# Kernel tuning notes

Hardware: AMD Instinct MI355X
Metric: run time of the kernel (lower is better)

## Reference

```python
import jax, jax.numpy as jnp
import numpy as np

S, B, D, H, DH = 1024, 4, 1024, 16, 64


def setup_inputs() -> dict:
    key = jax.random.key(0)
    ks = jax.random.split(key, 12)
    inp = {
        "query": jax.random.normal(ks[0], (S, B, D), dtype=jnp.float32),
        "key": jax.random.normal(ks[1], (S, B, D), dtype=jnp.float32),
        "value": jax.random.normal(ks[2], (S, B, D), dtype=jnp.float32),
        "key_mask": jax.random.randint(ks[3], (S, B), 0, 2, dtype=jnp.int32),
        # per-head stacked projection weights (original loops nn.Linear per head)
        "Wq": jax.random.normal(ks[4], (H, D, DH), dtype=jnp.float32) * 0.02,
        "bq": jnp.zeros((H, DH), dtype=jnp.float32),
        "Wk": jax.random.normal(ks[5], (H, D, DH), dtype=jnp.float32) * 0.02,
        "bk": jnp.zeros((H, DH), dtype=jnp.float32),
        "Wv": jax.random.normal(ks[6], (H, D, DH), dtype=jnp.float32) * 0.02,
        "bv": jnp.zeros((H, DH), dtype=jnp.float32),
        "Wo": jax.random.normal(ks[7], (H * DH, D), dtype=jnp.float32) * 0.02,
        "bo": jnp.zeros((D,), dtype=jnp.float32),
    }
    return inp


def reference(query, key, value, key_mask, Wq, bq, Wk, bk, Wv, bv, Wo, bo):
    # query/key/value: [S, B, D] (seq-major, matching torch einsum 'imk,jmk->imj')
    q = jnp.einsum('smd,hdk->smhk', query, Wq) + bq  # [Sq, B, H, DH]
    k = jnp.einsum('smd,hdk->smhk', key, Wk) + bk    # [Sk, B, H, DH]
    v = jnp.einsum('smd,hdk->smhk', value, Wv) + bv  # [Sk, B, H, DH]

    scale = 1.0 / jnp.sqrt(jnp.float32(DH))
    scores = jnp.einsum('imhk,jmhk->himj', q, k) * scale  # [H, Sq, B, Sk]
    # key_mask: [Sk, B] -> transpose -> [B, Sk]; additive -1e18 masking
    scores = scores - key_mask.astype(jnp.float32).T * 1e18
    attn = jax.nn.softmax(scores, axis=-1)
    out = jnp.einsum('himj,jmhk->imhk', attn, v)  # [Sq, B, H, DH]
    concat = out.reshape(out.shape[0], out.shape[1], H * DH)
    return concat @ Wo + bo  # [Sq, B, D]
```

## Files before the change

### kernel.cpp

```cpp
#include <hip/hip_runtime.h>
#include <hip/hip_bf16.h>


typedef __attribute__((ext_vector_type(8))) short short8;
typedef __attribute__((ext_vector_type(4))) short short4_;
typedef __attribute__((ext_vector_type(4))) float f32x4;
typedef __attribute__((ext_vector_type(16))) float f32x16;
typedef __attribute__((ext_vector_type(8))) __bf16 bf16x8;
typedef __attribute__((ext_vector_type(4))) __bf16 bf16x4;

union B8 {
    short8 s;
    bf16x8 b;
    unsigned short u[8];
};
union B4 {
    short4_ s;
    bf16x4 b;
    unsigned short u[4];
    int i[2];
};

#if __has_builtin(__builtin_amdgcn_exp2f)
#define EXP2(x) __builtin_amdgcn_exp2f(x)
#else
#define EXP2(x) exp2f(x)
#endif
#if __has_builtin(__builtin_amdgcn_rcpf)
#define RCP(x) __builtin_amdgcn_rcpf(x)
#else
#define RCP(x) (1.0f / (x))
#endif

static __device__ __forceinline__ unsigned short f2bf_rne(float f) {
    union { float f; unsigned u; } v; v.f = f;
    unsigned r = v.u + 0x7FFFu + ((v.u >> 16) & 1u);
    return (unsigned short)(r >> 16);
}

static __device__ __forceinline__ void async_lds16(const void* g, const void* l) {
    __builtin_amdgcn_global_load_lds(
        (const __attribute__((address_space(1))) unsigned int*)(unsigned long long)g,
        (__attribute__((address_space(3))) unsigned int*)(unsigned int)(unsigned long long)l,
        16, 0, 0);
}

__global__ __launch_bounds__(256) void prep(
    const float* __restrict__ Wq, const float* __restrict__ Wk,
    const float* __restrict__ Wv, const float* __restrict__ Wo,
    const float* __restrict__ query, const float* __restrict__ key,
    const float* __restrict__ value,
    unsigned short* __restrict__ WT,
    unsigned short* __restrict__ qA, unsigned short* __restrict__ kA,
    unsigned short* __restrict__ vA) {
    const int t = threadIdx.x;
    const int z = blockIdx.z;

    if (z >= 4) {
        const int zz = z - 4;
        const int tensor = zz >> 2;
        const int part = zz & 3;
        const float* src = (tensor == 0) ? query : (tensor == 1) ? key : value;
        unsigned short* dst = (tensor == 0) ? qA : (tensor == 1) ? kA : vA;
        const int blk = blockIdx.y * 16 + blockIdx.x;
        const size_t base = (size_t)part * 1048576 + (size_t)blk * 4096 + t * 16;
        B8 w0, w1;
#pragma unroll
        for (int i = 0; i < 2; ++i) {
            f32x4 a = *(const f32x4*)(src + base + i * 8);
            f32x4 b = *(const f32x4*)(src + base + i * 8 + 4);
#pragma unroll
            for (int j = 0; j < 4; ++j) {
                (i ? w1 : w0).u[j] = f2bf_rne(a[j]);
                (i ? w1 : w0).u[4 + j] = f2bf_rne(b[j]);
            }
        }
        *(short8*)(dst + base) = w0.s;
        *(short8*)(dst + base + 8) = w1.s;
        return;
    }

    __shared__ float sT[64][65];
    const int dtile = blockIdx.x;
    const int sub = blockIdx.y;
    const float* src;
    int spitch;
    unsigned short* dst;
    if (z < 3) {
        const float* W = (z == 0) ? Wq : (z == 1) ? Wk : Wv;
        src = W + (size_t)sub * 65536 + (size_t)dtile * 64 * 64;
        spitch = 64;
        dst = WT + (size_t)z * 1048576 + (size_t)(sub * 64) * 1024 + dtile * 64;
    } else {
        src = Wo + (size_t)dtile * 64 * 1024 + sub * 64;
        spitch = 1024;
        dst = WT + (size_t)3 * 1048576 + (size_t)(sub * 64) * 1024 + dtile * 64;
    }

    const int r = t >> 2;
    const int cseg = (t & 3) * 16;
#pragma unroll
    for (int i = 0; i < 4; ++i) {
        f32x4 v = *(const f32x4*)(src + (size_t)r * spitch + cseg + i * 4);
#pragma unroll
        for (int j = 0; j < 4; ++j) sT[r][cseg + i * 4 + j] = v[j];
    }
    __syncthreads();
    B8 w0, w1;
#pragma unroll
    for (int i = 0; i < 8; ++i) {
        w0.u[i] = f2bf_rne(sT[cseg + i][r]);
        w1.u[i] = f2bf_rne(sT[cseg + 8 + i][r]);
    }
    *(short8*)(dst + (size_t)r * 1024 + cseg) = w0.s;
    *(short8*)(dst + (size_t)r * 1024 + cseg + 8) = w1.s;
}

template <bool OUT_F32, bool BIAS_ROW>
__device__ __forceinline__ void gemm128(unsigned short* __restrict__ sA,
                                        unsigned short* __restrict__ sB,
                                        const unsigned short* __restrict__ A,
                                        size_t lda,
                                        const unsigned short* __restrict__ Bt,
                                        size_t ldb,
                                        const float* __restrict__ bias,
                                        void* __restrict__ Cv, size_t ldc,
                                        float oscale, int row0, int col0) {
    const int t = threadIdx.x;
    const int w = t >> 6;
    const int lane = t & 63;
    const int quad = lane >> 4;
    const int l15 = lane & 15;
    const int wr = w >> 1;
    const int wc = w & 1;
    const int srow16 = lane >> 2;
    const int sgseg = (lane & 3) ^ ((lane >> 3) & 3);
    const int rseg = (quad ^ ((l15 >> 1) & 3)) * 8;

    f32x4 acc[4][4] = {};

    const unsigned short* agp = A + (size_t)(row0 + w * 32 + srow16) * lda + sgseg * 8;
    const unsigned short* agp2 = agp + (size_t)16 * lda;
    const unsigned short* bgp = Bt + (size_t)(col0 + w * 32 + srow16) * ldb + sgseg * 8;
    const unsigned short* bgp2 = bgp + (size_t)16 * ldb;
    const int ldsA0 = (w * 32) * 32;
    const int ldsA1 = (w * 32 + 16) * 32;

    auto STAGE = [&](int tt, int off) {
        const int k0 = tt * 32;
        async_lds16(agp + k0, sA + off + ldsA0);
        async_lds16(agp2 + k0, sA + off + ldsA1);
        async_lds16(bgp + k0, sB + off + ldsA0);
        async_lds16(bgp2 + k0, sB + off + ldsA1);
    };
    auto COMPUTE = [&](int off) {
        const unsigned short* sac = sA + off;
        const unsigned short* sbc = sB + off;
        B8 af[4], bf[4];
#pragma unroll
        for (int i = 0; i < 4; ++i)
            af[i].s = *(const short8*)&sac[(wr * 64 + i * 16 + l15) * 32 + rseg];
#pragma unroll
        for (int j = 0; j < 4; ++j)
            bf[j].s = *(const short8*)&sbc[(wc * 64 + j * 16 + l15) * 32 + rseg];
#pragma unroll
        for (int i = 0; i < 4; ++i)
#pragma unroll
            for (int j = 0; j < 4; ++j)
                acc[i][j] = __builtin_amdgcn_mfma_f32_16x16x32_bf16(af[i].b, bf[j].b,
                                                                    acc[i][j], 0, 0, 0);
    };

    STAGE(0, 0);
    STAGE(1, 4096);

    for (int t3 = 0; t3 < 30; t3 += 3) {
        asm volatile("s_waitcnt vmcnt(4)" ::: "memory");
        __builtin_amdgcn_s_barrier();
        STAGE(t3 + 2, 8192);
        COMPUTE(0);
        asm volatile("s_waitcnt vmcnt(4)" ::: "memory");
        __builtin_amdgcn_s_barrier();
        STAGE(t3 + 3, 0);
        COMPUTE(4096);
        asm volatile("s_waitcnt vmcnt(4)" ::: "memory");
        __builtin_amdgcn_s_barrier();
        STAGE(t3 + 4, 4096);
        COMPUTE(8192);
    }
    asm volatile("s_waitcnt vmcnt(4)" ::: "memory");
    __builtin_amdgcn_s_barrier();
    COMPUTE(0);
    asm volatile("s_waitcnt vmcnt(0)" ::: "memory");
    __builtin_amdgcn_s_barrier();
    COMPUTE(4096);

    float brow[4][4];
    if constexpr (BIAS_ROW) {
#pragma unroll
        for (int i = 0; i < 4; ++i)
#pragma unroll
            for (int r = 0; r < 4; ++r)
                brow[i][r] = bias[row0 + wr * 64 + i * 16 + quad * 4 + r];
    }
#pragma unroll
    for (int j = 0; j < 4; ++j) {
        const int col = col0 + wc * 64 + j * 16 + l15;
        const float bcol = BIAS_ROW ? 0.0f : bias[col];
#pragma unroll
        for (int i = 0; i < 4; ++i) {
#pragma unroll
            for (int r = 0; r < 4; ++r) {
                const int row = row0 + wr * 64 + i * 16 + quad * 4 + r;
                const size_t idx = (size_t)row * ldc + col;
                const float bb = BIAS_ROW ? brow[i][r] : bcol;
                const float val = (acc[i][j][r] + bb) * oscale;
                if constexpr (OUT_F32)
                    ((float*)Cv)[idx] = val;
                else
                    ((unsigned short*)Cv)[idx] = f2bf_rne(val);
            }
        }
    }
}

#define SCALE_L2E 0.18033688011112042f

__global__ __launch_bounds__(256) void qkv_gemm(
    const unsigned short* __restrict__ qA, const unsigned short* __restrict__ kA,
    const unsigned short* __restrict__ vA,
    const unsigned short* __restrict__ WT,
    const float* __restrict__ bq, const float* __restrict__ bk, const float* __restrict__ bv,
    unsigned short* q_o, unsigned short* k_o, unsigned short* vT_o) {
    __shared__ unsigned short sA[3 * 128 * 32];
    __shared__ unsigned short sB[3 * 128 * 32];
    const int p = blockIdx.z;
    if (p < 2) {
        const unsigned short* A = (p == 0) ? qA : kA;
        const unsigned short* Bt = WT + (size_t)p * 1048576;
        const float* bias = (p == 0) ? bq : bk;
        unsigned short* C = (p == 0) ? q_o : k_o;
        const float osc = (p == 0) ? SCALE_L2E : 1.0f;
        gemm128<false, false>(sA, sB, A, 1024, Bt, 1024, bias, C, 1024, osc,
                              blockIdx.x * 128, blockIdx.y * 128);
    } else {
        const int b = blockIdx.x >> 3;
        const int rt = blockIdx.x & 7;
        gemm128<false, true>(sA, sB, WT + (size_t)2 * 1048576, 1024,
                             vA + (size_t)b * 1024, 4096, bv,
                             vT_o + (size_t)b * 1048576, 1024, 1.0f,
                             rt * 128, blockIdx.y * 128);
    }
}

__global__ __launch_bounds__(256) void out_gemm(const unsigned short* __restrict__ A,
                                                const unsigned short* __restrict__ WT,
                                                const float* __restrict__ bo,
                                                float* __restrict__ C) {
    __shared__ unsigned short sA[3 * 128 * 32];
    __shared__ unsigned short sB[3 * 128 * 32];
    gemm128<true, false>(sA, sB, A, 1024, WT + (size_t)3 * 1048576, 1024, bo, C, 1024,
                         1.0f, blockIdx.x * 128, blockIdx.y * 128);
}

#if __has_builtin(__builtin_amdgcn_mfma_f32_32x32x8bf16_1k)
#define HAVE_X8 1
#endif

__global__ __launch_bounds__(256) void attn_kernel(
    const unsigned short* __restrict__ q,
    const unsigned short* __restrict__ k,
    const unsigned short* __restrict__ vT,
    const int* __restrict__ key_mask,
    unsigned short* __restrict__ o) {
    __shared__ unsigned short sK[3 * 64 * 64];
    __shared__ unsigned short sVt[3 * 64 * 64];
    __shared__ float sBias[1024];
    __shared__ unsigned long long sBits[16];

    const int t = threadIdx.x;
    const int wave = t >> 6;
    const int lane = t & 63;
    const int n31 = lane & 31;
    const int hh = lane >> 5;
    const int n7 = n31 & 7;

    const int L = blockIdx.x + 8 * (blockIdx.y + 4 * blockIdx.z);
    const int xcd = L & 7;
    const int kk = L >> 3;
    const int g = (xcd << 3) | (kk >> 3);
    const int qt = kk & 7;
    const int b = g & 3;
    const int h = g >> 2;
    const int q0w = qt * 128 + wave * 32;

#pragma unroll
    for (int i = 0; i < 4; ++i) {
        const int idx = i * 4 + wave;
        const int sk = idx * 64 + lane;
        unsigned long long bal = __ballot(key_mask[sk * 4 + b] != 0);
        if (lane == 0) sBits[idx] = bal;
    }
    __syncthreads();
#pragma unroll
    for (int i = 0; i < 4; ++i) {
        const int idx = t * 4 + i;
        const int r = idx & 15;
        const int hb = (idx >> 4) & 1;
        const int blk = (idx >> 5) & 1;
        const int kt = idx >> 6;
        const int row = (r & 3) + 8 * (r >> 2) + 4 * hb + blk * 32;
        sBias[idx] = ((sBits[kt] >> row) & 1ull) ? -16384.0f : 0.0f;
    }

    bf16x8 qf[4];
    {
        const unsigned short* qrow =
            q + ((size_t)(q0w + n31) * 4 + b) * 1024 + h * 64 + hh * 8;
#pragma unroll
        for (int kc = 0; kc < 4; ++kc) {
            B8 tmp;
            tmp.s = *(const short8*)(qrow + kc * 16);
            qf[kc] = tmp.b;
        }
    }
    __syncthreads();

    f32x16 O0 = {}, O1 = {}, L_ = {};
    B4 ones;
#pragma unroll
    for (int j = 0; j < 4; ++j) ones.u[j] = 0x3F80;
#if !defined(HAVE_X8)
    B8 ones8;
#pragma unroll
    for (int j = 0; j < 8; ++j) ones8.u[j] = 0x3F80;
#endif

    const unsigned short* kbase = k + (size_t)b * 1024 + h * 64;
    const unsigned short* vtb = vT + ((size_t)(b * 16 + h) * 64) * 1024;

    const int lr8 = lane >> 3;
    const int gc = (lane & 7) ^ lr8;
    const unsigned short* kst0 = kbase + (size_t)(wave * 16 + lr8) * 4096 + gc * 8;
    const unsigned short* kst1 = kst0 + (size_t)8 * 4096;
    const unsigned short* vst0 = vtb + (size_t)(wave * 16 + lr8) * 1024 + gc * 8;
    const unsigned short* vst1 = vst0 + (size_t)8 * 1024;
    const int lds0 = (wave * 16) * 64;
    const int lds1 = (wave * 16 + 8) * 64;

    auto STAGE = [&](int tt, int boff) {
        const size_t k0 = (size_t)tt * 64;
        async_lds16(kst0 + k0 * 4096, sK + boff + lds0);
        async_lds16(kst1 + k0 * 4096, sK + boff + lds1);
        async_lds16(vst0 + k0, sVt + boff + lds0);
        async_lds16(vst1 + k0, sVt + boff + lds1);
    };

    auto ITER = [&](int kt, int curB, int stT, int stB, bool doStage, bool last) {
        if (last)
            asm volatile("s_waitcnt vmcnt(0)" ::: "memory");
        else
            asm volatile("s_waitcnt vmcnt(4)" ::: "memory");
        __builtin_amdgcn_s_barrier();
        if (doStage) STAGE(stT, stB);
        const unsigned short* sKc = sK + curB;
        const unsigned short* sVc = sVt + curB;
        B4 pfr[2][4];
#pragma unroll
        for (int blk = 0; blk < 2; ++blk) {
            f32x16 c;
            const f32x4* bp = (const f32x4*)&sBias[((kt * 2 + blk) * 2 + hh) * 16];
#pragma unroll
            for (int i = 0; i < 4; ++i) {
                f32x4 x = bp[i];
#pragma unroll
                for (int j = 0; j < 4; ++j) c[i * 4 + j] = x[j];
            }
            __builtin_amdgcn_s_setprio(1);
#pragma unroll
            for (int kc = 0; kc < 4; ++kc) {
                B8 af;
                af.s = *(const short8*)&sKc[(blk * 32 + n31) * 64 +
                                            (((kc * 2 + hh) ^ n7) << 3)];
                c = __builtin_amdgcn_mfma_f32_32x32x16_bf16(af.b, qf[kc], c, 0, 0, 0);
            }
            __builtin_amdgcn_s_setprio(0);
#pragma unroll
            for (int gg = 0; gg < 4; ++gg)
#pragma unroll
                for (int j = 0; j < 4; ++j)
                    pfr[blk][gg].b[j] = (__bf16)EXP2(c[gg * 4 + j]);
        }
#if defined(HAVE_X8)
        __builtin_amdgcn_s_setprio(1);
#pragma unroll
        for (int blk = 0; blk < 2; ++blk) {
#pragma unroll
            for (int gg = 0; gg < 4; ++gg) {
                const int sg = (((blk * 4 + gg) ^ n7) << 3) + hh * 4;
                B4 b0, b1;
                b0.s = *(const short4_*)&sVc[n31 * 64 + sg];
                b1.s = *(const short4_*)&sVc[(32 + n31) * 64 + sg];
                O0 = __builtin_amdgcn_mfma_f32_32x32x8bf16_1k(pfr[blk][gg].s, b0.s, O0, 0, 0, 0);
                O1 = __builtin_amdgcn_mfma_f32_32x32x8bf16_1k(pfr[blk][gg].s, b1.s, O1, 0, 0, 0);
                L_ = __builtin_amdgcn_mfma_f32_32x32x8bf16_1k(pfr[blk][gg].s, ones.s, L_, 0, 0, 0);
            }
        }
        __builtin_amdgcn_s_setprio(0);
#else
        __builtin_amdgcn_s_setprio(1);
#pragma unroll
        for (int blk = 0; blk < 2; ++blk) {
            B4 par[4];
#pragma unroll
            for (int gg = 0; gg < 4; ++gg) {
                par[gg].i[0] = __shfl_xor(pfr[blk][gg].i[0], 32);
                par[gg].i[1] = __shfl_xor(pfr[blk][gg].i[1], 32);
            }
#pragma unroll
            for (int w2 = 0; w2 < 2; ++w2) {
                const int gsel = 2 * w2 + hh;
                B4 lo = (hh == 0) ? pfr[blk][gsel] : par[gsel];
                B4 hi = (hh == 0) ? par[gsel] : pfr[blk][gsel];
                B8 afr;
#pragma unroll
                for (int j = 0; j < 4; ++j) {
                    afr.u[j] = lo.u[j];
                    afr.u[4 + j] = hi.u[j];
                }
                const int cg = blk * 4 + w2 * 2 + hh;
                const int sg = (cg ^ n7) << 3;
                B8 b0, b1;
                b0.s = *(const short8*)&sVc[n31 * 64 + sg];
                b1.s = *(const short8*)&sVc[(32 + n31) * 64 + sg];
                O0 = __builtin_amdgcn_mfma_f32_32x32x16_bf16(afr.b, b0.b, O0, 0, 0, 0);
                O1 = __builtin_amdgcn_mfma_f32_32x32x16_bf16(afr.b, b1.b, O1, 0, 0, 0);
                L_ = __builtin_amdgcn_mfma_f32_32x32x16_bf16(afr.b, ones8.b, L_, 0, 0, 0);
            }
        }
        __builtin_amdgcn_s_setprio(0);
#endif
    };

    STAGE(0, 0);
    STAGE(1, 4096);
    for (int t3 = 0; t3 < 12; t3 += 3) {
        ITER(t3, 0, t3 + 2, 8192, true, false);
        ITER(t3 + 1, 4096, t3 + 3, 0, true, false);
        ITER(t3 + 2, 8192, t3 + 4, 4096, true, false);
    }
    ITER(12, 0, 14, 8192, true, false);
    ITER(13, 4096, 15, 0, true, false);
    ITER(14, 8192, 0, 0, false, false);
    ITER(15, 0, 0, 0, false, true);

    unsigned short* obase = o + ((size_t)q0w * 4 + b) * 1024 + h * 64 + n31;
#pragma unroll
    for (int r = 0; r < 16; ++r) {
        const int qr = (r & 3) + 8 * (r >> 2) + 4 * hh;
        const float inv = RCP(L_[r]);
        obase[(size_t)qr * 4096] = f2bf_rne(O0[r] * inv);
        obase[(size_t)qr * 4096 + 32] = f2bf_rne(O1[r] * inv);
    }
}

extern "C" void kernel_launch(void* const* d_in, const int* in_sizes, int n_in,
                              void* d_out, int out_size, void* d_ws, size_t ws_size,
                              hipStream_t stream) {
    const float* query = (const float*)d_in[0];
    const float* key_ = (const float*)d_in[1];
    const float* value = (const float*)d_in[2];
    const int* key_mask = (const int*)d_in[3];
    const float* Wq = (const float*)d_in[4];
    const float* bq = (const float*)d_in[5];
    const float* Wk = (const float*)d_in[6];
    const float* bk = (const float*)d_in[7];
    const float* Wv = (const float*)d_in[8];
    const float* bv = (const float*)d_in[9];
    const float* Wo = (const float*)d_in[10];
    const float* bo = (const float*)d_in[11];
    float* out = (float*)d_out;

    const size_t NE = (size_t)4096 * 1024;
    unsigned short* q_ws = (unsigned short*)d_ws;
    unsigned short* k_ws = q_ws + NE;
    unsigned short* v_ws = k_ws + NE;
    unsigned short* a_ws = v_ws + NE;
    unsigned short* wt_ws = a_ws + NE;

    unsigned short* qA = a_ws;
    unsigned short* kA = (unsigned short*)d_out;
    unsigned short* vA = kA + NE;

    prep<<<dim3(16, 16, 16), 256, 0, stream>>>(Wq, Wk, Wv, Wo, query, key_, value,
                                               wt_ws, qA, kA, vA);
    qkv_gemm<<<dim3(32, 8, 3), 256, 0, stream>>>(qA, kA, vA, wt_ws,
                                                 bq, bk, bv, q_ws, k_ws, v_ws);
    attn_kernel<<<dim3(8, 4, 16), 256, 0, stream>>>(q_ws, k_ws, v_ws, key_mask, a_ws);
    out_gemm<<<dim3(32, 8, 1), 256, 0, stream>>>(a_ws, wt_ws, bo, out);
}
```

Baseline: 196.0 us.

## Process two 32-row query tiles per wave in attention with 128-thread blocks

```diff
diff --git a/kernel.cpp b/kernel.cpp
--- a/kernel.cpp
+++ b/kernel.cpp
@@ -267,7 +267,7 @@
 #define HAVE_X8 1
 #endif
 
-__global__ __launch_bounds__(256) void attn_kernel(
+__global__ __launch_bounds__(128, 2) void attn_kernel(
     const unsigned short* __restrict__ q,
     const unsigned short* __restrict__ k,
     const unsigned short* __restrict__ vT,
@@ -275,7 +275,7 @@
     unsigned short* __restrict__ o) {
     __shared__ unsigned short sK[3 * 64 * 64];
     __shared__ unsigned short sVt[3 * 64 * 64];
-    __shared__ float sBias[1024];
+    __shared__ unsigned int sMask[64];
     __shared__ unsigned long long sBits[16];
 
     const int t = threadIdx.x;
@@ -292,41 +292,46 @@
     const int qt = kk & 7;
     const int b = g & 3;
     const int h = g >> 2;
-    const int q0w = qt * 128 + wave * 32;
-
-#pragma unroll
-    for (int i = 0; i < 4; ++i) {
-        const int idx = i * 4 + wave;
+    const int qbase = qt * 128 + wave * 64;
+
+#pragma unroll
+    for (int i = 0; i < 8; ++i) {
+        const int idx = i * 2 + wave;
         const int sk = idx * 64 + lane;
         unsigned long long bal = __ballot(key_mask[sk * 4 + b] != 0);
         if (lane == 0) sBits[idx] = bal;
     }
     __syncthreads();
-#pragma unroll
-    for (int i = 0; i < 4; ++i) {
-        const int idx = t * 4 + i;
-        const int r = idx & 15;
-        const int hb = (idx >> 4) & 1;
-        const int blk = (idx >> 5) & 1;
-        const int kt = idx >> 6;
-        const int row = (r & 3) + 8 * (r >> 2) + 4 * hb + blk * 32;
-        sBias[idx] = ((sBits[kt] >> row) & 1ull) ? -16384.0f : 0.0f;
-    }
-
-    bf16x8 qf[4];
+    if (t < 64) {
+        const int kt = t >> 2;
+        const int hh2 = (t >> 1) & 1;
+        const int blk = t & 1;
+        unsigned int m = 0;
+#pragma unroll
+        for (int r = 0; r < 16; ++r) {
+            const int row = (r & 3) + 8 * (r >> 2) + 4 * hh2 + 32 * blk;
+            m |= ((unsigned int)((sBits[kt] >> row) & 1ull)) << r;
+        }
+        sMask[t] = m;
+    }
+
+    bf16x8 qfA[4], qfB[4];
     {
-        const unsigned short* qrow =
-            q + ((size_t)(q0w + n31) * 4 + b) * 1024 + h * 64 + hh * 8;
+        const unsigned short* qrowA =
+            q + ((size_t)(qbase + n31) * 4 + b) * 1024 + h * 64 + hh * 8;
+        const unsigned short* qrowB = qrowA + (size_t)32 * 4096;
 #pragma unroll
         for (int kc = 0; kc < 4; ++kc) {
-            B8 tmp;
-            tmp.s = *(const short8*)(qrow + kc * 16);
-            qf[kc] = tmp.b;
+            B8 ta, tb;
+            ta.s = *(const short8*)(qrowA + kc * 16);
+            tb.s = *(const short8*)(qrowB + kc * 16);
+            qfA[kc] = ta.b;
+            qfB[kc] = tb.b;
         }
     }
     __syncthreads();
 
-    f32x16 O0 = {}, O1 = {}, L_ = {};
+    f32x16 OA0 = {}, OA1 = {}, LA = {}, OB0 = {}, OB1 = {}, LB = {};
     B4 ones;
 #pragma unroll
     for (int j = 0; j < 4; ++j) ones.u[j] = 0x3F80;
@@ -341,40 +346,46 @@
 
     const int lr8 = lane >> 3;
     const int gc = (lane & 7) ^ lr8;
-    const unsigned short* kst0 = kbase + (size_t)(wave * 16 + lr8) * 4096 + gc * 8;
-    const unsigned short* kst1 = kst0 + (size_t)8 * 4096;
-    const unsigned short* vst0 = vtb + (size_t)(wave * 16 + lr8) * 1024 + gc * 8;
-    const unsigned short* vst1 = vst0 + (size_t)8 * 1024;
-    const int lds0 = (wave * 16) * 64;
-    const int lds1 = (wave * 16 + 8) * 64;
+    const int r0 = wave * 32;
+    const unsigned short* kst[4];
+    const unsigned short* vst[4];
+    int ldsc[4];
+#pragma unroll
+    for (int c = 0; c < 4; ++c) {
+        kst[c] = kbase + (size_t)(r0 + c * 8 + lr8) * 4096 + gc * 8;
+        vst[c] = vtb + (size_t)(r0 + c * 8 + lr8) * 1024 + gc * 8;
+        ldsc[c] = (r0 + c * 8) * 64;
+    }
 
     auto STAGE = [&](int tt, int boff) {
-        const size_t k0 = (size_t)tt * 64;
-        async_lds16(kst0 + k0 * 4096, sK + boff + lds0);
-        async_lds16(kst1 + k0 * 4096, sK + boff + lds1);
-        async_lds16(vst0 + k0, sVt + boff + lds0);
-        async_lds16(vst1 + k0, sVt + boff + lds1);
+        const size_t kk0 = (size_t)tt * 64;
+#pragma unroll
+        for (int c = 0; c < 4; ++c) {
+            async_lds16(kst[c] + kk0 * 4096, sK + boff + ldsc[c]);
+            async_lds16(vst[c] + kk0, sVt + boff + ldsc[c]);
+        }
     };
 
     auto ITER = [&](int kt, int curB, int stT, int stB, bool doStage, bool last) {
         if (last)
             asm volatile("s_waitcnt vmcnt(0)" ::: "memory");
         else
-            asm volatile("s_waitcnt vmcnt(4)" ::: "memory");
+            asm volatile("s_waitcnt vmcnt(8)" ::: "memory");
         __builtin_amdgcn_s_barrier();
         if (doStage) STAGE(stT, stB);
         const unsigned short* sKc = sK + curB;
         const unsigned short* sVc = sVt + curB;
-        B4 pfr[2][4];
+        const unsigned int* mp = &sMask[kt * 4 + hh * 2];
+        B4 pfrA[2][4], pfrB[2][4];
 #pragma unroll
         for (int blk = 0; blk < 2; ++blk) {
-            f32x16 c;
-            const f32x4* bp = (const f32x4*)&sBias[((kt * 2 + blk) * 2 + hh) * 16];
-#pragma unroll
-            for (int i = 0; i < 4; ++i) {
-                f32x4 x = bp[i];
-#pragma unroll
-                for (int j = 0; j < 4; ++j) c[i * 4 + j] = x[j];
+            const unsigned int mk = mp[blk];
+            f32x16 cA, cB;
+#pragma unroll
+            for (int r = 0; r < 16; ++r) {
+                const float bv2 = ((mk >> r) & 1u) ? -16384.0f : 0.0f;
+                cA[r] = bv2;
+                cB[r] = bv2;
             }
             __builtin_amdgcn_s_setprio(1);
 #pragma unroll
@@ -382,14 +393,17 @@
                 B8 af;
                 af.s = *(const short8*)&sKc[(blk * 32 + n31) * 64 +
                                             (((kc * 2 + hh) ^ n7) << 3)];
-                c = __builtin_amdgcn_mfma_f32_32x32x16_bf16(af.b, qf[kc], c, 0, 0, 0);
+                cA = __builtin_amdgcn_mfma_f32_32x32x16_bf16(af.b, qfA[kc], cA, 0, 0, 0);
+                cB = __builtin_amdgcn_mfma_f32_32x32x16_bf16(af.b, qfB[kc], cB, 0, 0, 0);
             }
             __builtin_amdgcn_s_setprio(0);
 #pragma unroll
             for (int gg = 0; gg < 4; ++gg)
 #pragma unroll
-                for (int j = 0; j < 4; ++j)
-                    pfr[blk][gg].b[j] = (__bf16)EXP2(c[gg * 4 + j]);
+                for (int j = 0; j < 4; ++j) {
+                    pfrA[blk][gg].b[j] = (__bf16)EXP2(cA[gg * 4 + j]);
+                    pfrB[blk][gg].b[j] = (__bf16)EXP2(cB[gg * 4 + j]);
+                }
         }
 #if defined(HAVE_X8)
         __builtin_amdgcn_s_setprio(1);
@@ -401,9 +415,12 @@
                 B4 b0, b1;
                 b0.s = *(const short4_*)&sVc[n31 * 64 + sg];
                 b1.s = *(const short4_*)&sVc[(32 + n31) * 64 + sg];
-                O0 = __builtin_amdgcn_mfma_f32_32x32x8bf16_1k(pfr[blk][gg].s, b0.s, O0, 0, 0, 0);
-                O1 = __builtin_amdgcn_mfma_f32_32x32x8bf16_1k(pfr[blk][gg].s, b1.s, O1, 0, 0, 0);
-                L_ = __builtin_amdgcn_mfma_f32_32x32x8bf16_1k(pfr[blk][gg].s, ones.s, L_, 0, 0, 0);
+                OA0 = __builtin_amdgcn_mfma_f32_32x32x8bf16_1k(pfrA[blk][gg].s, b0.s, OA0, 0, 0, 0);
+                OA1 = __builtin_amdgcn_mfma_f32_32x32x8bf16_1k(pfrA[blk][gg].s, b1.s, OA1, 0, 0, 0);
+                LA = __builtin_amdgcn_mfma_f32_32x32x8bf16_1k(pfrA[blk][gg].s, ones.s, LA, 0, 0, 0);
+                OB0 = __builtin_amdgcn_mfma_f32_32x32x8bf16_1k(pfrB[blk][gg].s, b0.s, OB0, 0, 0, 0);
+                OB1 = __builtin_amdgcn_mfma_f32_32x32x8bf16_1k(pfrB[blk][gg].s, b1.s, OB1, 0, 0, 0);
+                LB = __builtin_amdgcn_mfma_f32_32x32x8bf16_1k(pfrB[blk][gg].s, ones.s, LB, 0, 0, 0);
             }
         }
         __builtin_amdgcn_s_setprio(0);
@@ -411,31 +428,40 @@
         __builtin_amdgcn_s_setprio(1);
 #pragma unroll
         for (int blk = 0; blk < 2; ++blk) {
-            B4 par[4];
+            B4 parA[4], parB[4];
 #pragma unroll
             for (int gg = 0; gg < 4; ++gg) {
-                par[gg].i[0] = __shfl_xor(pfr[blk][gg].i[0], 32);
-                par[gg].i[1] = __shfl_xor(pfr[blk][gg].i[1], 32);
+                parA[gg].i[0] = __shfl_xor(pfrA[blk][gg].i[0], 32);
+                parA[gg].i[1] = __shfl_xor(pfrA[blk][gg].i[1], 32);
+                parB[gg].i[0] = __shfl_xor(pfrB[blk][gg].i[0], 32);
+                parB[gg].i[1] = __shfl_xor(pfrB[blk][gg].i[1], 32);
             }
 #pragma unroll
             for (int w2 = 0; w2 < 2; ++w2) {
                 const int gsel = 2 * w2 + hh;
-                B4 lo = (hh == 0) ? pfr[blk][gsel] : par[gsel];
-                B4 hi = (hh == 0) ? par[gsel] : pfr[blk][gsel];
-                B8 afr;
+                B4 loA = (hh == 0) ? pfrA[blk][gsel] : parA[gsel];
+                B4 hiA = (hh == 0) ? parA[gsel] : pfrA[blk][gsel];
+                B4 loB = (hh == 0) ? pfrB[blk][gsel] : parB[gsel];
+                B4 hiB = (hh == 0) ? parB[gsel] : pfrB[blk][gsel];
+                B8 afrA, afrB;
 #pragma unroll
                 for (int j = 0; j < 4; ++j) {
-                    afr.u[j] = lo.u[j];
-                    afr.u[4 + j] = hi.u[j];
+                    afrA.u[j] = loA.u[j];
+                    afrA.u[4 + j] = hiA.u[j];
+                    afrB.u[j] = loB.u[j];
+                    afrB.u[4 + j] = hiB.u[j];
                 }
                 const int cg = blk * 4 + w2 * 2 + hh;
                 const int sg = (cg ^ n7) << 3;
                 B8 b0, b1;
                 b0.s = *(const short8*)&sVc[n31 * 64 + sg];
                 b1.s = *(const short8*)&sVc[(32 + n31) * 64 + sg];
-                O0 = __builtin_amdgcn_mfma_f32_32x32x16_bf16(afr.b, b0.b, O0, 0, 0, 0);
-                O1 = __builtin_amdgcn_mfma_f32_32x32x16_bf16(afr.b, b1.b, O1, 0, 0, 0);
-                L_ = __builtin_amdgcn_mfma_f32_32x32x16_bf16(afr.b, ones8.b, L_, 0, 0, 0);
+                OA0 = __builtin_amdgcn_mfma_f32_32x32x16_bf16(afrA.b, b0.b, OA0, 0, 0, 0);
+                OA1 = __builtin_amdgcn_mfma_f32_32x32x16_bf16(afrA.b, b1.b, OA1, 0, 0, 0);
+                LA = __builtin_amdgcn_mfma_f32_32x32x16_bf16(afrA.b, ones8.b, LA, 0, 0, 0);
+                OB0 = __builtin_amdgcn_mfma_f32_32x32x16_bf16(afrB.b, b0.b, OB0, 0, 0, 0);
+                OB1 = __builtin_amdgcn_mfma_f32_32x32x16_bf16(afrB.b, b1.b, OB1, 0, 0, 0);
+                LB = __builtin_amdgcn_mfma_f32_32x32x16_bf16(afrB.b, ones8.b, LB, 0, 0, 0);
             }
         }
         __builtin_amdgcn_s_setprio(0);
@@ -454,13 +480,16 @@
     ITER(14, 8192, 0, 0, false, false);
     ITER(15, 0, 0, 0, false, true);
 
-    unsigned short* obase = o + ((size_t)q0w * 4 + b) * 1024 + h * 64 + n31;
+    unsigned short* obase = o + ((size_t)qbase * 4 + b) * 1024 + h * 64 + n31;
 #pragma unroll
     for (int r = 0; r < 16; ++r) {
         const int qr = (r & 3) + 8 * (r >> 2) + 4 * hh;
-        const float inv = RCP(L_[r]);
-        obase[(size_t)qr * 4096] = f2bf_rne(O0[r] * inv);
-        obase[(size_t)qr * 4096 + 32] = f2bf_rne(O1[r] * inv);
+        const float invA = RCP(LA[r]);
+        obase[(size_t)qr * 4096] = f2bf_rne(OA0[r] * invA);
+        obase[(size_t)qr * 4096 + 32] = f2bf_rne(OA1[r] * invA);
+        const float invB = RCP(LB[r]);
+        obase[(size_t)(qr + 32) * 4096] = f2bf_rne(OB0[r] * invB);
+        obase[(size_t)(qr + 32) * 4096 + 32] = f2bf_rne(OB1[r] * invB);
     }
 }
 
@@ -496,6 +525,6 @@
                                                wt_ws, qA, kA, vA);
     qkv_gemm<<<dim3(32, 8, 3), 256, 0, stream>>>(qA, kA, vA, wt_ws,
                                                  bq, bk, bv, q_ws, k_ws, v_ws);
-    attn_kernel<<<dim3(8, 4, 16), 256, 0, stream>>>(q_ws, k_ws, v_ws, key_mask, a_ws);
+    attn_kernel<<<dim3(8, 4, 16), 128, 0, stream>>>(q_ws, k_ws, v_ws, key_mask, a_ws);
     out_gemm<<<dim3(32, 8, 1), 256, 0, stream>>>(a_ws, wt_ws, bo, out);
 }
```

Result: slower. 220.9 us (+12.7%).
